# Performance work log

Measured on AMD Instinct MI355X. Metric: run time of the kernel, lower is better.

The kernel has to match this reference:

```python
import jax, jax.numpy as jnp
import numpy as np

K = 15.0          # sigmoid sharpness in get_approxi
THETA2 = 400.0    # gaussian 'theta2' parameter
LOSS_WEIGHT = 1.0


def obb2poly_le90(boxes):
    # boxes [..., 5] = (x, y, w, h, a) -> poly [..., 8]
    x, y, w, h, a = (boxes[..., i] for i in range(5))
    cosa, sina = jnp.cos(a), jnp.sin(a)
    wx, wy = 0.5 * w * cosa, 0.5 * w * sina
    hx, hy = -0.5 * h * sina, 0.5 * h * cosa
    return jnp.stack([
        x - wx - hx, y - wy - hy,
        x + wx - hx, y + wy - hy,
        x + wx + hx, y + wy + hy,
        x - wx + hx, y - wy + hy,
    ], axis=-1)


def setup_inputs() -> dict:
    key = jax.random.key(0)
    k1, k2, k3, k4, k5, k6 = jax.random.split(key, 6)
    N, M = 256, 512

    def make_boxes(k):
        u = jax.random.uniform(k, (N, 5), dtype=jnp.float32)
        cx = 100.0 + 300.0 * u[:, 0]
        cy = 100.0 + 300.0 * u[:, 1]
        w = 20.0 + 100.0 * u[:, 2]
        h = 20.0 + 100.0 * u[:, 3]
        a = (u[:, 4] - 0.5) * (jnp.pi / 2)
        return jnp.stack([cx, cy, w, h, a], axis=-1)

    pred = make_boxes(k1)
    target = make_boxes(k2)
    mask = 512.0 * jax.random.uniform(k3, (N, M, 2), dtype=jnp.float32)
    grad_x = jax.random.normal(k4, (N, M), dtype=jnp.float32)
    grad_y = jax.random.normal(k5, (N, M), dtype=jnp.float32)
    offset = 50.0 * jax.random.uniform(k6, (N, 2), dtype=jnp.float32)
    return {"pred": pred, "target": target, "mask": mask,
            "grad_x": grad_x, "grad_y": grad_y, "offset": offset}


def _my_loss(pred, target, mask, grad_x, grad_y, offset):
    # pred/target [N,5], mask [N,M,2], grad_x/grad_y [N,M], offset [N,2]
    px = pred[:, 0] - offset[:, 0]   # [N]
    py = pred[:, 1] - offset[:, 1]
    pw, ph, pa = pred[:, 2], pred[:, 3], pred[:, 4]
    gx = target[:, 0] - offset[:, 0]
    gy = target[:, 1] - offset[:, 1]
    gw, gh, ga = target[:, 2], target[:, 3], target[:, 4]

    mx, my = mask[..., 0], mask[..., 1]            # [N,M]
    dx = mx - gx[:, None]
    dy = my - gy[:, None]
    d = jnp.sqrt(dx * dx + dy * dy)                # [N,M]
    acos_arg = jnp.clip((gx[:, None] - mx) / d, -1.0, 1.0)
    acosv = jnp.arccos(acos_arg)
    beta = jnp.where(gy[:, None] >= my, ga[:, None] + acosv, ga[:, None] - acosv)

    d_w = jnp.abs(d * jnp.cos(beta))
    d_h = jnp.abs(d * jnp.sin(beta))
    sig = jax.nn.sigmoid
    approxi_1 = (1.0 - sig(K * (d_w - gw[:, None]) / gw[:, None])) * \
                (1.0 - sig(K * (d_h - gh[:, None]) / gh[:, None]))  # [N,M]

    d_w_p = pw[:, None] * d_w / gw[:, None]
    d_h_p = ph[:, None] * d_h / gh[:, None]
    zeros = jnp.zeros_like(d_w_p)
    boxes = jnp.stack([zeros, zeros, 2.0 * d_w_p, 2.0 * d_h_p,
                       jnp.broadcast_to(pa[:, None], d_w_p.shape)], axis=-1)
    pts = obb2poly_le90(boxes)                     # [N,M,8]

    half_pi = jnp.pi / 2
    q2 = (beta > -half_pi) & (beta <= 0.0)
    q3 = (beta > -jnp.pi) & (beta <= -half_pi)
    q4 = (beta > half_pi) & (beta <= jnp.pi)
    # default (q1: 0 < beta <= pi/2) -> corner 0
    gpx = jnp.where(q2, pts[..., 2], jnp.where(q3, pts[..., 4], jnp.where(q4, pts[..., 6], pts[..., 0])))
    gpy = jnp.where(q2, pts[..., 3], jnp.where(q3, pts[..., 5], jnp.where(q4, pts[..., 7], pts[..., 1])))
    guass_x = px[:, None] + gpx                    # [N,M]
    guass_y = py[:, None] + gpy

    # approxi_2[n,i,j] = exp(+||guass_i - mask_j||^2 / (2*theta2^2)) / (2*pi*theta2)
    dgx = guass_x[:, :, None] - mx[:, None, :]
    dgy = guass_y[:, :, None] - my[:, None, :]
    approxi_2 = jnp.exp((dgx * dgx + dgy * dgy) / (2.0 * THETA2 * THETA2)) / (2.0 * jnp.pi * THETA2)

    # w[n,i,j] = gx_i*gx_j + gy_i*gy_j
    w = grad_x[:, :, None] * grad_x[:, None, :] + grad_y[:, :, None] * grad_y[:, None, :]

    loss_per_box = jnp.mean(w * approxi_2 * approxi_1[:, None, :], axis=(1, 2))  # [N]
    return loss_per_box


def reference(pred, target, mask, grad_x, grad_y, offset):
    loss_per_box = _my_loss(pred, target, mask, grad_x, grad_y, offset)
    return LOSS_WEIGHT * jnp.mean(loss_per_box)  # reduction='mean'
```

## Files before the change

kernel.cpp:

```cpp
#include <hip/hip_runtime.h>
#include <math.h>

typedef float v2f __attribute__((ext_vector_type(2)));

#define N_BOX   256
#define M_PTS   512
#define S_SPLIT 8
#define BLK     64
#define R_ROWS  8
#define M2_PER  (M_PTS / S_SPLIT)
#define GRID    (N_BOX * S_SPLIT)

__global__ __launch_bounds__(BLK, 2) void loss_main(
    const float* __restrict__ pred,
    const float* __restrict__ target,
    const float* __restrict__ mask,
    const float* __restrict__ gradx,
    const float* __restrict__ grady,
    const float* __restrict__ offset,
    float* __restrict__ part)
{
    __shared__ float4 sPack[M2_PER];

    const int n = blockIdx.x >> 3;
    const int s = blockIdx.x & 7;
    const int t = threadIdx.x;

    const float offx = offset[n * 2 + 0];
    const float offy = offset[n * 2 + 1];
    const float px = pred[n * 5 + 0] - offx;
    const float py = pred[n * 5 + 1] - offy;
    const float pw = pred[n * 5 + 2];
    const float ph = pred[n * 5 + 3];
    const float pa = pred[n * 5 + 4];
    const float gx = target[n * 5 + 0] - offx;
    const float gy = target[n * 5 + 1] - offy;
    const float gw = target[n * 5 + 2];
    const float gh = target[n * 5 + 3];
    const float ga = target[n * 5 + 4];

    float sinpa, cospa, singa, cosga;
    sincosf(pa, &sinpa, &cospa);
    sincosf(ga, &singa, &cosga);

    const float THETA2   = 400.0f;
    const float LOG2E    = 1.4426950408889634f;
    const float c1       = LOG2E / (2.0f * THETA2 * THETA2);
    const float rs       = sqrtf(c1);
    const float inv_norm = 1.0f / (2.0f * (float)M_PI * THETA2);

    const float pwg = pw / gw, phg = ph / gh;
    const float cwx = pwg * cospa, swx = pwg * sinpa;
    const float chx = phg * cospa, shx = phg * sinpa;
    const float absinga = fabsf(singa);
    const float kA  = 15.0f * LOG2E / gw;
    const float kH  = 15.0f * LOG2E / gh;
    const float kB  = 15.0f * LOG2E;
    const float pxrs = px * rs, pyrs = py * rs;
    const bool  gaPos = (ga > 0.0f), gaNeg = (ga < 0.0f);

    const float2* mask2 = (const float2*)mask;
    const size_t  baseM = (size_t)n * M_PTS;

    v2f Gx[4], Gy[4], gvx2[4], gvy2[4];

#pragma unroll
    for (int r = 0; r < R_ROWS; ++r) {
        const int    m  = t + (r << 6);
        const float2 mp = mask2[baseM + m];
        const float dx = mp.x - gx;
        const float dy = mp.y - gy;
        const float u = singa * dy - cosga * dx;
        const float v = -(cosga * dy + singa * dx);
        const bool sgaOk = gaPos ? (dy <= 0.0f) : (gaNeg ? (dy > 0.0f) : false);
        const bool wrap  = sgaOk && (dx > 0.0f) && (dx * absinga > fabsf(dy) * cosga);
        const float au = fabsf(u), av = fabsf(v);
        const float dws = (wrap || v > 0.0f) ? -au : au;
        const float dhs = (wrap || u > 0.0f) ? -av : av;
        const float gpx = dws * cwx - dhs * shx;
        const float gpy = dws * swx + dhs * chx;
        const float gvx = gradx[baseM + m];
        const float gvy = grady[baseM + m];
        Gx[r >> 1][r & 1]   = fmaf(gpx, rs, pxrs);
        Gy[r >> 1][r & 1]   = fmaf(gpy, rs, pyrs);
        gvx2[r >> 1][r & 1] = gvx;
        gvy2[r >> 1][r & 1] = gvy;
        if (r == s) {
            const float eA = __builtin_amdgcn_exp2f(fmaf(au, kA, -kB));
            const float eB = __builtin_amdgcn_exp2f(fmaf(av, kH, -kB));
            const float B  = inv_norm / ((1.0f + eA) * (1.0f + eB));
            sPack[t] = make_float4(mp.x * rs, mp.y * rs, gvx * B, gvy * B);
        }
    }
    __syncthreads();

    v2f accz[4], accw[4];
#pragma unroll
    for (int q = 0; q < 4; ++q) { accz[q] = (v2f)0.0f; accw[q] = (v2f)0.0f; }

#pragma unroll 4
    for (int m2 = 0; m2 < M2_PER; ++m2) {
        const float4 p = sPack[m2];
#pragma unroll
        for (int q = 0; q < 4; ++q) {
            v2f dgx = Gx[q] - p.x;
            v2f dgy = Gy[q] - p.y;
            v2f sa  = dgx * dgx + dgy * dgy;
            v2f e;
            e.x = __builtin_amdgcn_exp2f(sa.x);
            e.y = __builtin_amdgcn_exp2f(sa.y);
            accz[q] += e * p.z;
            accw[q] += e * p.w;
        }
    }

    v2f tot2 = accz[0] * gvx2[0] + accw[0] * gvy2[0];
    tot2 += accz[1] * gvx2[1] + accw[1] * gvy2[1];
    tot2 += accz[2] * gvx2[2] + accw[2] * gvy2[2];
    tot2 += accz[3] * gvx2[3] + accw[3] * gvy2[3];
    float acc = tot2.x + tot2.y;

#pragma unroll
    for (int off = 32; off > 0; off >>= 1)
        acc += __shfl_down(acc, off, 64);
    if (t == 0) part[blockIdx.x] = acc;
}

__global__ __launch_bounds__(256) void loss_reduce(const float* __restrict__ part,
                                                   float* __restrict__ out)
{
    __shared__ float sW[4];
    const int t = threadIdx.x;
    const float4* p4 = (const float4*)part;
    const float4 a = p4[t];
    const float4 b = p4[t + 256];
    float acc = ((a.x + a.y) + (a.z + a.w)) + ((b.x + b.y) + (b.z + b.w));
#pragma unroll
    for (int off = 32; off > 0; off >>= 1)
        acc += __shfl_down(acc, off, 64);
    if ((t & 63) == 0) sW[t >> 6] = acc;
    __syncthreads();
    if (t == 0) {
        const float scale = 1.0f / ((float)N_BOX * (float)M_PTS * (float)M_PTS);
        out[0] = (sW[0] + sW[1] + sW[2] + sW[3]) * scale;
    }
}

extern "C" void kernel_launch(void* const* d_in, const int* in_sizes, int n_in,
                              void* d_out, int out_size, void* d_ws, size_t ws_size,
                              hipStream_t stream) {
    const float* pred   = (const float*)d_in[0];
    const float* target = (const float*)d_in[1];
    const float* mask   = (const float*)d_in[2];
    const float* gradx  = (const float*)d_in[3];
    const float* grady  = (const float*)d_in[4];
    const float* offset = (const float*)d_in[5];
    float* out  = (float*)d_out;
    float* part = (float*)d_ws;

    hipLaunchKernelGGL(loss_main, dim3(GRID), dim3(BLK), 0, stream,
                       pred, target, mask, gradx, grady, offset, part);
    hipLaunchKernelGGL(loss_reduce, dim3(1), dim3(256), 0, stream, part, out);
}
```

Before: 81.23 us.

## Expand squared distance into FMAs and split mask columns across more blocks

The inner loop now expands the squared distance as |G|^2 - 2G·m + |m|^2. The |m|^2 term is folded as an exp2 factor into the per-column weights in shared memory, and the -2c1*G and c1*|G|^2 terms are precomputed per row, so each pair costs two FMAs plus exp2 instead of subtracts and squares. The column split is doubled to 16 blocks per box with 32 columns each, and the launch bound is raised to 4 blocks per CU to improve latency hiding. The expansion adds large cancelling terms, which may lose float precision, and the finer split adds per-block setup and more partial sums.

Result: no change. 81.50 us (+0.3%).

```diff
diff --git a/kernel.cpp b/kernel.cpp
--- a/kernel.cpp
+++ b/kernel.cpp
@@ -1,17 +1,15 @@
 #include <hip/hip_runtime.h>
 #include <math.h>
 
-typedef float v2f __attribute__((ext_vector_type(2)));
-
 #define N_BOX   256
 #define M_PTS   512
-#define S_SPLIT 8
+#define S_SPLIT 16
 #define BLK     64
 #define R_ROWS  8
 #define M2_PER  (M_PTS / S_SPLIT)
 #define GRID    (N_BOX * S_SPLIT)
 
-__global__ __launch_bounds__(BLK, 2) void loss_main(
+__global__ __launch_bounds__(BLK, 4) void loss_main(
     const float* __restrict__ pred,
     const float* __restrict__ target,
     const float* __restrict__ mask,
@@ -22,8 +20,8 @@
 {
     __shared__ float4 sPack[M2_PER];
 
-    const int n = blockIdx.x >> 3;
-    const int s = blockIdx.x & 7;
+    const int n = blockIdx.x >> 4;
+    const int s = blockIdx.x & 15;
     const int t = threadIdx.x;
 
     const float offx = offset[n * 2 + 0];
@@ -46,7 +44,7 @@
     const float THETA2   = 400.0f;
     const float LOG2E    = 1.4426950408889634f;
     const float c1       = LOG2E / (2.0f * THETA2 * THETA2);
-    const float rs       = sqrtf(c1);
+    const float n2c1     = -2.0f * c1;
     const float inv_norm = 1.0f / (2.0f * (float)M_PI * THETA2);
 
     const float pwg = pw / gw, phg = ph / gh;
@@ -56,14 +54,15 @@
     const float kA  = 15.0f * LOG2E / gw;
     const float kH  = 15.0f * LOG2E / gh;
     const float kB  = 15.0f * LOG2E;
-    const float pxrs = px * rs, pyrs = py * rs;
     const bool  gaPos = (ga > 0.0f), gaNeg = (ga < 0.0f);
 
     const float2* mask2 = (const float2*)mask;
     const size_t  baseM = (size_t)n * M_PTS;
 
-    v2f Gx[4], Gy[4], gvx2[4], gvy2[4];
+    float Gx2[R_ROWS], Gy2[R_ROWS], nG[R_ROWS], gvxr[R_ROWS], gvyr[R_ROWS];
 
+    const int  rStore = s >> 1;
+    const bool tMatch = ((t >> 5) == (s & 1));
 #pragma unroll
     for (int r = 0; r < R_ROWS; ++r) {
         const int    m  = t + (r << 6);
@@ -77,48 +76,46 @@
         const float au = fabsf(u), av = fabsf(v);
         const float dws = (wrap || v > 0.0f) ? -au : au;
         const float dhs = (wrap || u > 0.0f) ? -av : av;
-        const float gpx = dws * cwx - dhs * shx;
-        const float gpy = dws * swx + dhs * chx;
+        const float Gx = px + dws * cwx - dhs * shx;
+        const float Gy = py + dws * swx + dhs * chx;
         const float gvx = gradx[baseM + m];
         const float gvy = grady[baseM + m];
-        Gx[r >> 1][r & 1]   = fmaf(gpx, rs, pxrs);
-        Gy[r >> 1][r & 1]   = fmaf(gpy, rs, pyrs);
-        gvx2[r >> 1][r & 1] = gvx;
-        gvy2[r >> 1][r & 1] = gvy;
-        if (r == s) {
+        Gx2[r]  = n2c1 * Gx;
+        Gy2[r]  = n2c1 * Gy;
+        nG[r]   = c1 * fmaf(Gx, Gx, Gy * Gy);
+        gvxr[r] = gvx;
+        gvyr[r] = gvy;
+        if (tMatch && r == rStore) {
             const float eA = __builtin_amdgcn_exp2f(fmaf(au, kA, -kB));
             const float eB = __builtin_amdgcn_exp2f(fmaf(av, kH, -kB));
-            const float B  = inv_norm / ((1.0f + eA) * (1.0f + eB));
-            sPack[t] = make_float4(mp.x * rs, mp.y * rs, gvx * B, gvy * B);
+            const float m2n = c1 * fmaf(mp.x, mp.x, mp.y * mp.y);
+            const float B  = inv_norm * __builtin_amdgcn_exp2f(m2n)
+                             / ((1.0f + eA) * (1.0f + eB));
+            sPack[t & 31] = make_float4(mp.x, mp.y, gvx * B, gvy * B);
         }
     }
     __syncthreads();
 
-    v2f accz[4], accw[4];
+    float az[R_ROWS], aw[R_ROWS];
 #pragma unroll
-    for (int q = 0; q < 4; ++q) { accz[q] = (v2f)0.0f; accw[q] = (v2f)0.0f; }
+    for (int r = 0; r < R_ROWS; ++r) { az[r] = 0.0f; aw[r] = 0.0f; }
 
 #pragma unroll 4
     for (int m2 = 0; m2 < M2_PER; ++m2) {
         const float4 p = sPack[m2];
 #pragma unroll
-        for (int q = 0; q < 4; ++q) {
-            v2f dgx = Gx[q] - p.x;
-            v2f dgy = Gy[q] - p.y;
-            v2f sa  = dgx * dgx + dgy * dgy;
-            v2f e;
-            e.x = __builtin_amdgcn_exp2f(sa.x);
-            e.y = __builtin_amdgcn_exp2f(sa.y);
-            accz[q] += e * p.z;
-            accw[q] += e * p.w;
+        for (int r = 0; r < R_ROWS; ++r) {
+            const float sv = fmaf(Gx2[r], p.x, fmaf(Gy2[r], p.y, nG[r]));
+            const float e  = __builtin_amdgcn_exp2f(sv);
+            az[r] = fmaf(e, p.z, az[r]);
+            aw[r] = fmaf(e, p.w, aw[r]);
         }
     }
 
-    v2f tot2 = accz[0] * gvx2[0] + accw[0] * gvy2[0];
-    tot2 += accz[1] * gvx2[1] + accw[1] * gvy2[1];
-    tot2 += accz[2] * gvx2[2] + accw[2] * gvy2[2];
-    tot2 += accz[3] * gvx2[3] + accw[3] * gvy2[3];
-    float acc = tot2.x + tot2.y;
+    float acc = 0.0f;
+#pragma unroll
+    for (int r = 0; r < R_ROWS; ++r)
+        acc += fmaf(gvxr[r], az[r], gvyr[r] * aw[r]);
 
 #pragma unroll
     for (int off = 32; off > 0; off >>= 1)
@@ -132,9 +129,12 @@
     __shared__ float sW[4];
     const int t = threadIdx.x;
     const float4* p4 = (const float4*)part;
-    const float4 a = p4[t];
-    const float4 b = p4[t + 256];
-    float acc = ((a.x + a.y) + (a.z + a.w)) + ((b.x + b.y) + (b.z + b.w));
+    float acc = 0.0f;
+#pragma unroll
+    for (int j = 0; j < 4; ++j) {
+        const float4 a = p4[t + 256 * j];
+        acc += ((a.x + a.y) + (a.z + a.w));
+    }
 #pragma unroll
     for (int off = 32; off > 0; off >>= 1)
         acc += __shfl_down(acc, off, 64);
```
